# Kernel optimization log

Hardware: AMD Instinct MI355X
Metric: run time of the kernel (lower is better)

The kernel has to match this reference:

```python
import jax, jax.numpy as jnp
import numpy as np

B, N, E, D, STEPS = 32, 512, 4, 128, 5  # batch, n_node, n_edge_types, state_dim, n_steps


def setup_inputs() -> dict:
    key = jax.random.key(0)
    ks = jax.random.split(key, 16)
    s = 0.05  # xavier-ish scale for weights
    inp = {
        "prop_state": jax.random.normal(ks[0], (B, N, D), jnp.float32),
        # dense adjacency [B, N, 2*N*E]; scale by 1/(N) to keep bmm sums O(1)
        "A": jax.random.uniform(ks[1], (B, N, 2 * N * E), jnp.float32) * (2.0 / N),
        "node_mask": jnp.ones((B, N), dtype=jnp.int32),
        # per-edge-type in/out linears (applied orientation: x @ W + b)
        "in_W": jax.random.normal(ks[2], (E, D, D), jnp.float32) * s,
        "in_b": jax.random.normal(ks[3], (E, D), jnp.float32) * 1e-4,
        "out_W": jax.random.normal(ks[4], (E, D, D), jnp.float32) * s,
        "out_b": jax.random.normal(ks[5], (E, D), jnp.float32) * 1e-4,
        # GRU-style gates: Linear(3D -> D)
        "rW": jax.random.normal(ks[6], (3 * D, D), jnp.float32) * s,
        "rb": jax.random.normal(ks[7], (D,), jnp.float32) * 1e-4,
        "zW": jax.random.normal(ks[8], (3 * D, D), jnp.float32) * s,
        "zb": jax.random.normal(ks[9], (D,), jnp.float32) * 1e-4,
        "tW": jax.random.normal(ks[10], (3 * D, D), jnp.float32) * s,
        "tb": jax.random.normal(ks[11], (D,), jnp.float32) * 1e-4,
        # out_mlp: Linear(2D -> D) (dropout p=0 / eval mode -> identity)
        "oW": jax.random.normal(ks[12], (2 * D, D), jnp.float32) * s,
        "ob": jax.random.normal(ks[13], (D,), jnp.float32) * 1e-4,
    }
    return inp


def reference(prop_state, A, node_mask, in_W, in_b, out_W, out_b,
              rW, rb, zW, zb, tW, tb, oW, ob):
    del node_mask  # accepted but unused by GGNN.forward
    init_state = prop_state
    A_in = A[:, :, : N * E]    # [B, N, N*E]
    A_out = A[:, :, N * E:]    # [B, N, N*E]
    state = prop_state         # [B, N, D]
    for _ in range(STEPS):
        # per-edge-type linears, stacked edge-type-major: [B, E, N, D] -> [B, E*N, D]
        in_states = (jnp.einsum('bnd,edh->benh', state, in_W)
                     + in_b[None, :, None, :]).reshape(B, E * N, D)
        out_states = (jnp.einsum('bnd,edh->benh', state, out_W)
                      + out_b[None, :, None, :]).reshape(B, E * N, D)
        a_in = jnp.einsum('bnm,bmd->bnd', A_in, in_states)    # [B, N, D]
        a_out = jnp.einsum('bnm,bmd->bnd', A_out, out_states)  # [B, N, D]
        a = jnp.concatenate([a_in, a_out, state], axis=2)      # [B, N, 3D]
        r = jax.nn.sigmoid(a @ rW + rb)
        z = jax.nn.sigmoid(a @ zW + zb)
        joined = jnp.concatenate([a_in, a_out, r * state], axis=2)
        h_hat = jnp.tanh(joined @ tW + tb)
        state = (1.0 - z) * state + z * h_hat
    join_state = jnp.concatenate([state, init_state], axis=2)  # [B, N, 2D]
    return jnp.tanh(join_state @ oW + ob)                      # [B, N, D]
```

## Files before the change

### kernel.cpp

```cpp
#include <hip/hip_runtime.h>

#define DEV __device__ __forceinline__

using half8   = __attribute__((ext_vector_type(8))) _Float16;
using ushort8 = __attribute__((ext_vector_type(8))) unsigned short;
using f32x4   = __attribute__((ext_vector_type(4))) float;

typedef unsigned short ushort_t;

constexpr int B_ = 32, N_ = 512, E_ = 4, D_ = 128;
constexpr int NE = N_ * E_;
constexpr int M_TOT = B_ * N_;
constexpr int STEPS_ = 5;

DEV ushort_t f2h(float x) { union { _Float16 h; ushort_t u; } v; v.h = (_Float16)x; return v.u; }
DEV float sigmoidf_(float x) { return 1.0f / (1.0f + __expf(-x)); }

template<int ROWS>
DEV void stage64(const ushort_t* __restrict__ g, int ld, ushort_t* lds, int tid) {
    constexpr int TOT = ROWS * 8;
    static_assert(TOT % 256 == 0, "");
    int w = tid >> 6, lane = tid & 63;
#pragma unroll
    for (int c0 = 0; c0 < TOT; c0 += 256) {
        int c  = c0 + (w << 6) + lane;
        int r  = c >> 3;
        int cc = c & 7;
        __builtin_amdgcn_global_load_lds(
            (__attribute__((address_space(1))) void*)(g + r * ld + cc * 8),
            (__attribute__((address_space(3))) void*)(lds + (c0 + (w << 6)) * 8),
            16, 0, 0);
    }
}

template<int BM, int BN>
DEV void mma64(const ushort_t* lA, const ushort_t* lB,
               f32x4 (&acc)[BM/32][BN/32], int wm, int wn, int l15, int lg) {
    constexpr int MF = BM / 32, NF = BN / 32;
#pragma unroll
    for (int kk = 0; kk < 2; ++kk) {
        half8 a[MF], b[NF];
#pragma unroll
        for (int i = 0; i < MF; ++i)
            a[i] = *reinterpret_cast<const half8*>(lA + (wm*(BM/2) + i*16 + l15)*64 + kk*32 + lg*8);
#pragma unroll
        for (int j = 0; j < NF; ++j)
            b[j] = *reinterpret_cast<const half8*>(lB + (wn*(BN/2) + j*16 + l15)*64 + kk*32 + lg*8);
#pragma unroll
        for (int i = 0; i < MF; ++i)
#pragma unroll
            for (int j = 0; j < NF; ++j)
                acc[i][j] = __builtin_amdgcn_mfma_f32_16x16x32_f16(a[i], b[j], acc[i][j], 0, 0, 0);
    }
}

__global__ __launch_bounds__(256) void convertA_rs(const float* __restrict__ A,
                                                   ushort_t* __restrict__ A_h,
                                                   float* __restrict__ Ars) {
    int row = blockIdx.x, t = threadIdx.x;
    const float* src = A + (size_t)row * 4096 + t * 16;
    ushort_t* dst = A_h + (size_t)row * 4096 + t * 16;
    float s = 0.f;
#pragma unroll
    for (int c = 0; c < 2; ++c) {
        float4 v0 = reinterpret_cast<const float4*>(src)[2*c];
        float4 v1 = reinterpret_cast<const float4*>(src)[2*c+1];
        s += v0.x+v0.y+v0.z+v0.w + v1.x+v1.y+v1.z+v1.w;
        ushort8 r;
        r[0]=f2h(v0.x); r[1]=f2h(v0.y); r[2]=f2h(v0.z); r[3]=f2h(v0.w);
        r[4]=f2h(v1.x); r[5]=f2h(v1.y); r[6]=f2h(v1.z); r[7]=f2h(v1.w);
        *reinterpret_cast<ushort8*>(dst + 8*c) = r;
    }
#pragma unroll
    for (int m = 16; m; m >>= 1) s += __shfl_xor(s, m);
    if ((t & 31) == 0) Ars[(size_t)row * 8 + (t >> 5)] = s;
}

__global__ __launch_bounds__(256) void prep_weights(
    const float* __restrict__ in_W, const float* __restrict__ out_W,
    const float* __restrict__ rW, const float* __restrict__ zW,
    const float* __restrict__ tW, const float* __restrict__ oW,
    ushort_t* WstT, ushort_t* WrzT, ushort_t* WtT, ushort_t* WoT) {
    int idx = blockIdx.x * 256 + threadIdx.x;
    if (idx < 131072) {
        int io = idx >> 16, r = idx & 65535, d = r >> 9, eh = r & 511, e = eh >> 7, h = eh & 127;
        const float* W = io ? out_W : in_W;
        WstT[idx] = f2h(W[e*16384 + h*128 + d]);
        return;
    }
    idx -= 131072;
    if (idx < 98304) {
        int j = idx / 384, k = idx % 384;
        WrzT[idx] = f2h(j < 128 ? rW[k*128 + j] : zW[k*128 + (j-128)]);
        return;
    }
    idx -= 98304;
    if (idx < 49152) { int j = idx / 384, k = idx % 384; WtT[idx] = f2h(tW[k*128 + j]); return; }
    idx -= 49152;
    if (idx < 32768) { int j = idx / 256, k = idx % 256; WoT[idx] = f2h(oW[k*128 + j]); return; }
}

__global__ __launch_bounds__(256) void initState(const float* __restrict__ p,
                                                 float* __restrict__ sf,
                                                 ushort_t* __restrict__ sh,
                                                 ushort_t* __restrict__ ih) {
    int i = blockIdx.x * 256 + threadIdx.x;
    float4 v = reinterpret_cast<const float4*>(p)[i];
    reinterpret_cast<float4*>(sf)[i] = v;
    using u4 = __attribute__((ext_vector_type(4))) unsigned short;
    u4 r; r[0]=f2h(v.x); r[1]=f2h(v.y); r[2]=f2h(v.z); r[3]=f2h(v.w);
    *reinterpret_cast<u4*>(sh + 4*i) = r;
    *reinterpret_cast<u4*>(ih + 4*i) = r;
}

__global__ __launch_bounds__(256) void transT_kernel(const ushort_t* __restrict__ sh,
                                                     ushort_t* __restrict__ stateT) {
    __shared__ alignas(16) ushort_t trb[128 * 136];
    int tid = threadIdx.x, b = blockIdx.x >> 2, n0 = (blockIdx.x & 3) * 128;
#pragma unroll
    for (int rep = 0; rep < 8; ++rep) {
        int idx = rep * 256 + tid, r = idx >> 4, c8 = idx & 15;
        uint4 v = *reinterpret_cast<const uint4*>(sh + ((size_t)(b*512 + n0 + r))*128 + c8*8);
        *reinterpret_cast<uint4*>(trb + r*136 + c8*8) = v;
    }
    __syncthreads();
    int d = tid >> 1, half = tid & 1;
    ushort_t* dst = stateT + (size_t)b * 65536 + d * 512 + n0 + half * 64;
#pragma unroll
    for (int g = 0; g < 8; ++g) {
        ushort8 v;
#pragma unroll
        for (int k = 0; k < 8; ++k) v[k] = trb[(half*64 + g*8 + k)*136 + d];
        *reinterpret_cast<ushort8*>(dst + g*8) = v;
    }
}

__global__ __launch_bounds__(256) void bigG_kernel(const ushort_t* __restrict__ A_h,
                                                   const ushort_t* __restrict__ stateT,
                                                   ushort_t* __restrict__ G) {
    __shared__ alignas(16) ushort_t lA[128*64];
    __shared__ alignas(16) ushort_t lB[128*64];
    int tid = threadIdx.x, w = tid >> 6, l15 = tid & 15, lg = (tid & 63) >> 4;
    int wm = w >> 1, wn = w & 1;
    int bx = blockIdx.x;
    int bid = (bx & 7) * 128 + (bx >> 3);
    int nt = bid & 3, e = (bid >> 2) & 3, io = (bid >> 4) & 1, b = bid >> 5;

    const ushort_t* Asrc = A_h + ((size_t)(b*512 + nt*128))*4096 + io*2048 + e*512;
    const ushort_t* Bsrc = stateT + (size_t)b * 65536;
    ushort_t* Out = G + ((size_t)(b*512 + nt*128))*1024 + io*512 + e*128;

    f32x4 acc[4][4] = {};
    for (int k0 = 0; k0 < 512; k0 += 64) {
        stage64<128>(Asrc + k0, 4096, lA, tid);
        stage64<128>(Bsrc + k0, 512, lB, tid);
        __syncthreads();
        mma64<128, 128>(lA, lB, acc, wm, wn, l15, lg);
        __syncthreads();
    }
#pragma unroll
    for (int j = 0; j < 4; ++j) {
        int col = wn*64 + j*16 + l15;
#pragma unroll
        for (int i = 0; i < 4; ++i)
#pragma unroll
            for (int q = 0; q < 4; ++q) {
                int row = wm*64 + i*16 + lg*4 + q;
                Out[(size_t)row * 1024 + col] = f2h(acc[i][j][q]);
            }
    }
}

__global__ __launch_bounds__(256) void applyW_kernel(const ushort_t* __restrict__ G,
                                                     const ushort_t* __restrict__ WstT,
                                                     const float* __restrict__ Ars,
                                                     const float* __restrict__ in_b,
                                                     const float* __restrict__ out_b,
                                                     ushort_t* __restrict__ a_in_h,
                                                     ushort_t* __restrict__ a_out_h) {
    __shared__ alignas(16) ushort_t lA[128*64];
    __shared__ alignas(16) ushort_t lB[128*64];
    int tid = threadIdx.x, w = tid >> 6, l15 = tid & 15, lg = (tid & 63) >> 4;
    int wm = w >> 1, wn = w & 1;
    int mt = blockIdx.x >> 1, io = blockIdx.x & 1;

    const ushort_t* Asrc = G + (size_t)(mt*128)*1024 + io*512;
    const ushort_t* Bsrc = WstT + io * 65536;
    const float* bio = io ? out_b : in_b;
    ushort_t* Out = (io ? a_out_h : a_in_h);

    f32x4 acc[4][4] = {};
    for (int k0 = 0; k0 < 512; k0 += 64) {
        stage64<128>(Asrc + k0, 1024, lA, tid);
        stage64<128>(Bsrc + k0, 512, lB, tid);
        __syncthreads();
        mma64<128, 128>(lA, lB, acc, wm, wn, l15, lg);
        __syncthreads();
    }
#pragma unroll
    for (int j = 0; j < 4; ++j) {
        int col = wn*64 + j*16 + l15;
        float b0 = bio[col], b1 = bio[128+col], b2 = bio[256+col], b3 = bio[384+col];
#pragma unroll
        for (int i = 0; i < 4; ++i)
#pragma unroll
            for (int q = 0; q < 4; ++q) {
                int row = mt*128 + wm*64 + i*16 + lg*4 + q;
                float4 rs = *reinterpret_cast<const float4*>(Ars + (size_t)row*8 + io*4);
                float v = acc[i][j][q] + rs.x*b0 + rs.y*b1 + rs.z*b2 + rs.w*b3;
                Out[(size_t)row * 128 + col] = f2h(v);
            }
    }
}

__global__ __launch_bounds__(256) void rz_kernel(const ushort_t* __restrict__ a_in_h,
                                                 const ushort_t* __restrict__ a_out_h,
                                                 const ushort_t* __restrict__ state_h,
                                                 const ushort_t* __restrict__ WrzT,
                                                 const float* __restrict__ rb,
                                                 const float* __restrict__ zb,
                                                 const float* __restrict__ state_f32,
                                                 ushort_t* __restrict__ rsh,
                                                 float* __restrict__ z_f32) {
    __shared__ alignas(16) ushort_t lA[128*64];
    __shared__ alignas(16) ushort_t lB[128*64];
    int tid = threadIdx.x, w = tid >> 6, l15 = tid & 15, lg = (tid & 63) >> 4;
    int wm = w >> 1, wn = w & 1;
    int mt = blockIdx.x >> 1, cb = blockIdx.x & 1;

    const ushort_t* srcs[3] = { a_in_h + (size_t)mt*128*128,
                                a_out_h + (size_t)mt*128*128,
                                state_h + (size_t)mt*128*128 };
    const ushort_t* Bsrc = WrzT + (size_t)cb * 128 * 384;

    f32x4 acc[4][4] = {};
    for (int k0 = 0; k0 < 384; k0 += 64) {
        stage64<128>(srcs[k0 >> 7] + (k0 & 127), 128, lA, tid);
        stage64<128>(Bsrc + k0, 384, lB, tid);
        __syncthreads();
        mma64<128, 128>(lA, lB, acc, wm, wn, l15, lg);
        __syncthreads();
    }
    const float* bias = cb ? zb : rb;
#pragma unroll
    for (int j = 0; j < 4; ++j) {
        int col = wn*64 + j*16 + l15;
        float bv = bias[col];
#pragma unroll
        for (int i = 0; i < 4; ++i)
#pragma unroll
            for (int q = 0; q < 4; ++q) {
                int row = mt*128 + wm*64 + i*16 + lg*4 + q;
                size_t idx = (size_t)row * 128 + col;
                float g = sigmoidf_(acc[i][j][q] + bv);
                if (cb == 0) rsh[idx] = f2h(g * state_f32[idx]);
                else         z_f32[idx] = g;
            }
    }
}

__global__ __launch_bounds__(256) void t_kernel(const ushort_t* __restrict__ a_in_h,
                                                const ushort_t* __restrict__ a_out_h,
                                                const ushort_t* __restrict__ rsh,
                                                const ushort_t* __restrict__ WtT,
                                                const float* __restrict__ tb,
                                                const float* __restrict__ z_f32,
                                                float* __restrict__ state_f32,
                                                ushort_t* __restrict__ state_h,
                                                ushort_t* __restrict__ stateT) {
    __shared__ alignas(16) ushort_t sbuf[128 * 136];
    ushort_t* lA = sbuf;
    ushort_t* lB = sbuf + 8192;
    int tid = threadIdx.x, w = tid >> 6, l15 = tid & 15, lg = (tid & 63) >> 4;
    int wm = w >> 1, wn = w & 1;
    int mt = blockIdx.x;

    const ushort_t* srcs[3] = { a_in_h + (size_t)mt*128*128,
                                a_out_h + (size_t)mt*128*128,
                                rsh + (size_t)mt*128*128 };
    f32x4 acc[4][4] = {};
    for (int k0 = 0; k0 < 384; k0 += 64) {
        stage64<128>(srcs[k0 >> 7] + (k0 & 127), 128, lA, tid);
        stage64<128>(WtT + k0, 384, lB, tid);
        __syncthreads();
        mma64<128, 128>(lA, lB, acc, wm, wn, l15, lg);
        __syncthreads();
    }
#pragma unroll
    for (int j = 0; j < 4; ++j) {
        int col = wn*64 + j*16 + l15;
        float bv = tb[col];
#pragma unroll
        for (int i = 0; i < 4; ++i)
#pragma unroll
            for (int q = 0; q < 4; ++q) {
                int lrow = wm*64 + i*16 + lg*4 + q;
                int row = mt*128 + lrow;
                size_t idx = (size_t)row * 128 + col;
                float h = tanhf(acc[i][j][q] + bv);
                float z = z_f32[idx];
                float ns = (1.0f - z) * state_f32[idx] + z * h;
                state_f32[idx] = ns;
                ushort_t nh = f2h(ns);
                state_h[idx] = nh;
                sbuf[lrow * 136 + col] = nh;
            }
    }
    __syncthreads();
    int b = mt >> 2, n0 = (mt & 3) * 128;
    int d = tid >> 1, half = tid & 1;
    ushort_t* dst = stateT + (size_t)b * 65536 + d * 512 + n0 + half * 64;
#pragma unroll
    for (int g = 0; g < 8; ++g) {
        ushort8 v;
#pragma unroll
        for (int k = 0; k < 8; ++k) v[k] = sbuf[(half*64 + g*8 + k)*136 + d];
        *reinterpret_cast<ushort8*>(dst + g*8) = v;
    }
}

__global__ __launch_bounds__(256) void final_kernel(const ushort_t* __restrict__ state_h,
                                                    const ushort_t* __restrict__ init_h,
                                                    const ushort_t* __restrict__ WoT,
                                                    const float* __restrict__ ob,
                                                    float* __restrict__ out) {
    __shared__ alignas(16) ushort_t lA[128*64];
    __shared__ alignas(16) ushort_t lB[128*64];
    int tid = threadIdx.x, w = tid >> 6, l15 = tid & 15, lg = (tid & 63) >> 4;
    int wm = w >> 1, wn = w & 1;
    int mt = blockIdx.x;

    const ushort_t* srcs[2] = { state_h + (size_t)mt*128*128,
                                init_h + (size_t)mt*128*128 };
    f32x4 acc[4][4] = {};
    for (int k0 = 0; k0 < 256; k0 += 64) {
        stage64<128>(srcs[k0 >> 7] + (k0 & 127), 128, lA, tid);
        stage64<128>(WoT + k0, 256, lB, tid);
        __syncthreads();
        mma64<128, 128>(lA, lB, acc, wm, wn, l15, lg);
        __syncthreads();
    }
#pragma unroll
    for (int j = 0; j < 4; ++j) {
        int col = wn*64 + j*16 + l15;
        float bv = ob[col];
#pragma unroll
        for (int i = 0; i < 4; ++i)
#pragma unroll
            for (int q = 0; q < 4; ++q) {
                int row = mt*128 + wm*64 + i*16 + lg*4 + q;
                out[(size_t)row * 128 + col] = tanhf(acc[i][j][q] + bv);
            }
    }
}

extern "C" void kernel_launch(void* const* d_in, const int* in_sizes, int n_in,
                              void* d_out, int out_size, void* d_ws, size_t ws_size,
                              hipStream_t stream) {
    const float* prop  = (const float*)d_in[0];
    const float* A     = (const float*)d_in[1];
    const float* in_W  = (const float*)d_in[3];
    const float* in_b  = (const float*)d_in[4];
    const float* out_W = (const float*)d_in[5];
    const float* out_b = (const float*)d_in[6];
    const float* rW    = (const float*)d_in[7];
    const float* rb    = (const float*)d_in[8];
    const float* zW    = (const float*)d_in[9];
    const float* zb    = (const float*)d_in[10];
    const float* tW    = (const float*)d_in[11];
    const float* tb    = (const float*)d_in[12];
    const float* oW    = (const float*)d_in[13];
    const float* ob    = (const float*)d_in[14];
    float* outp = (float*)d_out;

    size_t off = 0;
    auto carve = [&](size_t bytes) {
        void* p = (char*)d_ws + off;
        off += (bytes + 255) & ~(size_t)255;
        return p;
    };
    ushort_t* A_h      = (ushort_t*)carve((size_t)M_TOT*4096*2);
    ushort_t* G        = (ushort_t*)carve((size_t)M_TOT*1024*2);
    ushort_t* stateT   = (ushort_t*)carve((size_t)B_*D_*N_*2);
    ushort_t* a_in_h   = (ushort_t*)carve((size_t)M_TOT*D_*2);
    ushort_t* a_out_h  = (ushort_t*)carve((size_t)M_TOT*D_*2);
    ushort_t* rsh      = (ushort_t*)carve((size_t)M_TOT*D_*2);
    ushort_t* state_h  = (ushort_t*)carve((size_t)M_TOT*D_*2);
    ushort_t* init_h   = (ushort_t*)carve((size_t)M_TOT*D_*2);
    float*    state_f32= (float*)carve((size_t)M_TOT*D_*4);
    float*    z_f32    = (float*)carve((size_t)M_TOT*D_*4);
    float*    Ars      = (float*)carve((size_t)M_TOT*8*4);
    ushort_t* WstT     = (ushort_t*)carve((size_t)2*128*512*2);
    ushort_t* WrzT     = (ushort_t*)carve((size_t)256*384*2);
    ushort_t* WtT      = (ushort_t*)carve((size_t)128*384*2);
    ushort_t* WoT      = (ushort_t*)carve((size_t)128*256*2);
    (void)ws_size; (void)n_in; (void)in_sizes; (void)out_size;

    convertA_rs<<<16384, 256, 0, stream>>>(A, A_h, Ars);
    prep_weights<<<1216, 256, 0, stream>>>(in_W, out_W, rW, zW, tW, oW, WstT, WrzT, WtT, WoT);
    initState<<<2048, 256, 0, stream>>>(prop, state_f32, state_h, init_h);
    transT_kernel<<<128, 256, 0, stream>>>(state_h, stateT);

    for (int s = 0; s < STEPS_; ++s) {
        bigG_kernel<<<1024, 256, 0, stream>>>(A_h, stateT, G);
        applyW_kernel<<<256, 256, 0, stream>>>(G, WstT, Ars, in_b, out_b, a_in_h, a_out_h);
        rz_kernel<<<256, 256, 0, stream>>>(a_in_h, a_out_h, state_h, WrzT, rb, zb,
                                           state_f32, rsh, z_f32);
        t_kernel<<<128, 256, 0, stream>>>(a_in_h, a_out_h, rsh, WtT, tb, z_f32,
                                          state_f32, state_h, stateT);
    }
    final_kernel<<<128, 256, 0, stream>>>(state_h, init_h, WoT, ob, outp);
}
```

Measured before the change: 998.9 us.

## Fuse applyW, rz and t stages into one GRU kernel with LDS-resident intermediates

Merges the per-step applyW, rz and t kernels into a single gru_kernel that handles 64-row tiles. a_in, a_out and r*state stay in swizzled LDS instead of going through global memory, and z is held in registers. It also fuses initState with the transpose, and stages bigG's output through LDS so global stores are coalesced. This cuts launches and global round-trips but uses 72KB of LDS per block, runs only 256 blocks, and has the smaller tile re-read the weight tiles more often.

Result: faster. 832.2 us (-16.7%).

```diff
diff --git a/kernel.cpp b/kernel.cpp
--- a/kernel.cpp
+++ b/kernel.cpp
@@ -33,25 +33,41 @@
     }
 }
 
-template<int BM, int BN>
-DEV void mma64(const ushort_t* lA, const ushort_t* lB,
-               f32x4 (&acc)[BM/32][BN/32], int wm, int wn, int l15, int lg) {
-    constexpr int MF = BM / 32, NF = BN / 32;
+DEV void st_swz(ushort_t* base, int row, int col, ushort_t v) {
+    int off = ((row * 128 + col) * 2) ^ ((row & 7) << 4);
+    *reinterpret_cast<ushort_t*>(reinterpret_cast<char*>(base) + off) = v;
+}
+
+template<int BM, int BN, int LDA, bool SWZ>
+DEV void mmaT(const ushort_t* lA, int k0, const ushort_t* lB,
+              f32x4 (&acc)[BM/32][BN/32], int wm, int wn, int l15, int lg) {
+    constexpr int MF = BM/32, NF = BN/32;
 #pragma unroll
     for (int kk = 0; kk < 2; ++kk) {
         half8 a[MF], b[NF];
 #pragma unroll
-        for (int i = 0; i < MF; ++i)
-            a[i] = *reinterpret_cast<const half8*>(lA + (wm*(BM/2) + i*16 + l15)*64 + kk*32 + lg*8);
+        for (int i = 0; i < MF; ++i) {
+            int row = wm*(BM/2) + i*16 + l15;
+            int off = (row*LDA + k0 + kk*32 + lg*8) * 2;
+            if (SWZ) off ^= (row & 7) << 4;
+            a[i] = *reinterpret_cast<const half8*>(reinterpret_cast<const char*>(lA) + off);
+        }
 #pragma unroll
         for (int j = 0; j < NF; ++j)
-            b[j] = *reinterpret_cast<const half8*>(lB + (wn*(BN/2) + j*16 + l15)*64 + kk*32 + lg*8);
+            b[j] = *reinterpret_cast<const half8*>(lB + (wn*(BN/2)+j*16+l15)*64 + kk*32 + lg*8);
 #pragma unroll
         for (int i = 0; i < MF; ++i)
 #pragma unroll
             for (int j = 0; j < NF; ++j)
                 acc[i][j] = __builtin_amdgcn_mfma_f32_16x16x32_f16(a[i], b[j], acc[i][j], 0, 0, 0);
     }
+}
+
+DEV void zacc(f32x4 (&acc)[2][4]) {
+#pragma unroll
+    for (int i = 0; i < 2; ++i)
+#pragma unroll
+        for (int j = 0; j < 4; ++j) acc[i][j] = (f32x4){0.f,0.f,0.f,0.f};
 }
 
 __global__ __launch_bounds__(256) void convertA_rs(const float* __restrict__ A,
@@ -100,46 +116,46 @@
     if (idx < 32768) { int j = idx / 256, k = idx % 256; WoT[idx] = f2h(oW[k*128 + j]); return; }
 }
 
-__global__ __launch_bounds__(256) void initState(const float* __restrict__ p,
-                                                 float* __restrict__ sf,
-                                                 ushort_t* __restrict__ sh,
-                                                 ushort_t* __restrict__ ih) {
-    int i = blockIdx.x * 256 + threadIdx.x;
-    float4 v = reinterpret_cast<const float4*>(p)[i];
-    reinterpret_cast<float4*>(sf)[i] = v;
-    using u4 = __attribute__((ext_vector_type(4))) unsigned short;
-    u4 r; r[0]=f2h(v.x); r[1]=f2h(v.y); r[2]=f2h(v.z); r[3]=f2h(v.w);
-    *reinterpret_cast<u4*>(sh + 4*i) = r;
-    *reinterpret_cast<u4*>(ih + 4*i) = r;
-}
-
-__global__ __launch_bounds__(256) void transT_kernel(const ushort_t* __restrict__ sh,
-                                                     ushort_t* __restrict__ stateT) {
-    __shared__ alignas(16) ushort_t trb[128 * 136];
-    int tid = threadIdx.x, b = blockIdx.x >> 2, n0 = (blockIdx.x & 3) * 128;
-#pragma unroll
-    for (int rep = 0; rep < 8; ++rep) {
-        int idx = rep * 256 + tid, r = idx >> 4, c8 = idx & 15;
-        uint4 v = *reinterpret_cast<const uint4*>(sh + ((size_t)(b*512 + n0 + r))*128 + c8*8);
-        *reinterpret_cast<uint4*>(trb + r*136 + c8*8) = v;
+__global__ __launch_bounds__(256) void initPlus(const float* __restrict__ p,
+                                                float* __restrict__ sf,
+                                                ushort_t* __restrict__ sh,
+                                                ushort_t* __restrict__ ih,
+                                                ushort_t* __restrict__ stateT) {
+    __shared__ ushort_t trb[128 * 132];
+    int tid = threadIdx.x, mt = blockIdx.x;
+    size_t base = (size_t)mt * 128 * 128;
+#pragma unroll
+    for (int rep = 0; rep < 16; ++rep) {
+        int idx = rep * 256 + tid, row = idx >> 5, c4 = idx & 31;
+        size_t o = base + (size_t)row * 128 + c4 * 4;
+        float4 v = *reinterpret_cast<const float4*>(p + o);
+        *reinterpret_cast<float4*>(sf + o) = v;
+        using u4 = __attribute__((ext_vector_type(4))) unsigned short;
+        u4 r; r[0]=f2h(v.x); r[1]=f2h(v.y); r[2]=f2h(v.z); r[3]=f2h(v.w);
+        *reinterpret_cast<u4*>(sh + o) = r;
+        *reinterpret_cast<u4*>(ih + o) = r;
+        trb[row*132 + c4*4 + 0] = r[0]; trb[row*132 + c4*4 + 1] = r[1];
+        trb[row*132 + c4*4 + 2] = r[2]; trb[row*132 + c4*4 + 3] = r[3];
     }
     __syncthreads();
-    int d = tid >> 1, half = tid & 1;
-    ushort_t* dst = stateT + (size_t)b * 65536 + d * 512 + n0 + half * 64;
-#pragma unroll
-    for (int g = 0; g < 8; ++g) {
+    int b = mt >> 2, n0 = (mt & 3) * 128, d = tid >> 1, half = tid & 1;
+    ushort_t* dst = stateT + (size_t)b * 65536 + (size_t)d * 512 + n0 + half * 64;
+#pragma unroll
+    for (int g2 = 0; g2 < 8; ++g2) {
         ushort8 v;
 #pragma unroll
-        for (int k = 0; k < 8; ++k) v[k] = trb[(half*64 + g*8 + k)*136 + d];
-        *reinterpret_cast<ushort8*>(dst + g*8) = v;
+        for (int k = 0; k < 8; ++k) v[k] = trb[(half*64 + g2*8 + k)*132 + d];
+        *reinterpret_cast<ushort8*>(dst + g2*8) = v;
     }
 }
 
 __global__ __launch_bounds__(256) void bigG_kernel(const ushort_t* __restrict__ A_h,
                                                    const ushort_t* __restrict__ stateT,
                                                    ushort_t* __restrict__ G) {
-    __shared__ alignas(16) ushort_t lA[128*64];
-    __shared__ alignas(16) ushort_t lB[128*64];
+    __shared__ char smem[128*136*2] __attribute__((aligned(16)));
+    ushort_t* sA  = (ushort_t*)smem;
+    ushort_t* sB  = (ushort_t*)(smem + 16384);
+    ushort_t* buf = (ushort_t*)smem;
     int tid = threadIdx.x, w = tid >> 6, l15 = tid & 15, lg = (tid & 63) >> 4;
     int wm = w >> 1, wn = w & 1;
     int bx = blockIdx.x;
@@ -152,10 +168,10 @@
 
     f32x4 acc[4][4] = {};
     for (int k0 = 0; k0 < 512; k0 += 64) {
-        stage64<128>(Asrc + k0, 4096, lA, tid);
-        stage64<128>(Bsrc + k0, 512, lB, tid);
+        stage64<128>(Asrc + k0, 4096, sA, tid);
+        stage64<128>(Bsrc + k0, 512, sB, tid);
         __syncthreads();
-        mma64<128, 128>(lA, lB, acc, wm, wn, l15, lg);
+        mmaT<128, 128, 64, false>(sA, 0, sB, acc, wm, wn, l15, lg);
         __syncthreads();
     }
 #pragma unroll
@@ -166,157 +182,168 @@
 #pragma unroll
             for (int q = 0; q < 4; ++q) {
                 int row = wm*64 + i*16 + lg*4 + q;
-                Out[(size_t)row * 1024 + col] = f2h(acc[i][j][q]);
+                buf[row*136 + col] = f2h(acc[i][j][q]);
             }
     }
-}
-
-__global__ __launch_bounds__(256) void applyW_kernel(const ushort_t* __restrict__ G,
-                                                     const ushort_t* __restrict__ WstT,
-                                                     const float* __restrict__ Ars,
-                                                     const float* __restrict__ in_b,
-                                                     const float* __restrict__ out_b,
-                                                     ushort_t* __restrict__ a_in_h,
-                                                     ushort_t* __restrict__ a_out_h) {
-    __shared__ alignas(16) ushort_t lA[128*64];
-    __shared__ alignas(16) ushort_t lB[128*64];
+    __syncthreads();
+#pragma unroll
+    for (int rep = 0; rep < 8; ++rep) {
+        int idx = rep*256 + tid, row = idx >> 4, c8 = idx & 15;
+        uint4 v = *reinterpret_cast<uint4*>(buf + row*136 + c8*8);
+        *reinterpret_cast<uint4*>(Out + (size_t)row*1024 + c8*8) = v;
+    }
+}
+
+__global__ __launch_bounds__(256, 2) void gru_kernel(
+    const ushort_t* __restrict__ G, const ushort_t* __restrict__ WstT,
+    const float* __restrict__ Ars, const float* __restrict__ in_b,
+    const float* __restrict__ out_b,
+    const ushort_t* __restrict__ WrzT, const float* __restrict__ rb,
+    const float* __restrict__ zb,
+    const ushort_t* __restrict__ WtT, const float* __restrict__ tb,
+    float* __restrict__ state_f32, ushort_t* __restrict__ state_h,
+    ushort_t* __restrict__ stateT) {
+    __shared__ char smem[73728] __attribute__((aligned(16)));
+    ushort_t* sA    = (ushort_t*)smem;
+    ushort_t* sB    = (ushort_t*)(smem + 8192);
+    ushort_t* a_in  = (ushort_t*)(smem + 24576);
+    ushort_t* a_out = (ushort_t*)(smem + 40960);
+    ushort_t* rsb   = (ushort_t*)(smem + 57344);
+    ushort_t* trb   = (ushort_t*)smem;
+
     int tid = threadIdx.x, w = tid >> 6, l15 = tid & 15, lg = (tid & 63) >> 4;
     int wm = w >> 1, wn = w & 1;
-    int mt = blockIdx.x >> 1, io = blockIdx.x & 1;
-
-    const ushort_t* Asrc = G + (size_t)(mt*128)*1024 + io*512;
-    const ushort_t* Bsrc = WstT + io * 65536;
-    const float* bio = io ? out_b : in_b;
-    ushort_t* Out = (io ? a_out_h : a_in_h);
-
-    f32x4 acc[4][4] = {};
-    for (int k0 = 0; k0 < 512; k0 += 64) {
-        stage64<128>(Asrc + k0, 1024, lA, tid);
-        stage64<128>(Bsrc + k0, 512, lB, tid);
-        __syncthreads();
-        mma64<128, 128>(lA, lB, acc, wm, wn, l15, lg);
-        __syncthreads();
-    }
+    int grow0 = blockIdx.x * 64;
+
+    f32x4 acc[2][4];
+    f32x4 zr[2][4];
+
+#define GRU_KSTEP_GLB(APTR, ALD, BPTR, BLD) do {                         \
+        stage64<64>((APTR), (ALD), sA, tid);                             \
+        stage64<128>((BPTR), (BLD), sB, tid);                            \
+        __syncthreads();                                                 \
+        mmaT<64,128,64,false>(sA, 0, sB, acc, wm, wn, l15, lg);          \
+        __syncthreads(); } while (0)
+
+#define GRU_KSTEP_LDS(ABASE, K0, BPTR, BLD) do {                         \
+        stage64<128>((BPTR), (BLD), sB, tid);                            \
+        __syncthreads();                                                 \
+        mmaT<64,128,128,true>((ABASE), (K0), sB, acc, wm, wn, l15, lg);  \
+        __syncthreads(); } while (0)
+
+    for (int io = 0; io < 2; ++io) {
+        zacc(acc);
+        for (int k0 = 0; k0 < 512; k0 += 64) {
+            GRU_KSTEP_GLB(G + (size_t)grow0*1024 + io*512 + k0, 1024,
+                          WstT + io*65536 + k0, 512);
+        }
+        const float* bio = io ? out_b : in_b;
+        ushort_t* adst = io ? a_out : a_in;
+#pragma unroll
+        for (int j = 0; j < 4; ++j) {
+            int col = wn*64 + j*16 + l15;
+            float b0 = bio[col], b1 = bio[128+col], b2 = bio[256+col], b3 = bio[384+col];
+#pragma unroll
+            for (int i = 0; i < 2; ++i)
+#pragma unroll
+                for (int q = 0; q < 4; ++q) {
+                    int row = wm*32 + i*16 + lg*4 + q;
+                    float4 rsv = *reinterpret_cast<const float4*>(Ars + (size_t)(grow0+row)*8 + io*4);
+                    float v = acc[i][j][q] + rsv.x*b0 + rsv.y*b1 + rsv.z*b2 + rsv.w*b3;
+                    st_swz(adst, row, col, f2h(v));
+                }
+        }
+    }
+
+    zacc(acc);
+    GRU_KSTEP_LDS(a_in,  0,  WrzT + 0,   384);
+    GRU_KSTEP_LDS(a_in,  64, WrzT + 64,  384);
+    GRU_KSTEP_LDS(a_out, 0,  WrzT + 128, 384);
+    GRU_KSTEP_LDS(a_out, 64, WrzT + 192, 384);
+    GRU_KSTEP_GLB(state_h + (size_t)grow0*128,      128, WrzT + 256, 384);
+    GRU_KSTEP_GLB(state_h + (size_t)grow0*128 + 64, 128, WrzT + 320, 384);
 #pragma unroll
     for (int j = 0; j < 4; ++j) {
         int col = wn*64 + j*16 + l15;
-        float b0 = bio[col], b1 = bio[128+col], b2 = bio[256+col], b3 = bio[384+col];
-#pragma unroll
-        for (int i = 0; i < 4; ++i)
+        float rbv = rb[col];
+#pragma unroll
+        for (int i = 0; i < 2; ++i)
 #pragma unroll
             for (int q = 0; q < 4; ++q) {
-                int row = mt*128 + wm*64 + i*16 + lg*4 + q;
-                float4 rs = *reinterpret_cast<const float4*>(Ars + (size_t)row*8 + io*4);
-                float v = acc[i][j][q] + rs.x*b0 + rs.y*b1 + rs.z*b2 + rs.w*b3;
-                Out[(size_t)row * 128 + col] = f2h(v);
+                int row = wm*32 + i*16 + lg*4 + q;
+                size_t idx = (size_t)(grow0+row)*128 + col;
+                float rg = sigmoidf_(acc[i][j][q] + rbv);
+                st_swz(rsb, row, col, f2h(rg * state_f32[idx]));
             }
     }
-}
-
-__global__ __launch_bounds__(256) void rz_kernel(const ushort_t* __restrict__ a_in_h,
-                                                 const ushort_t* __restrict__ a_out_h,
-                                                 const ushort_t* __restrict__ state_h,
-                                                 const ushort_t* __restrict__ WrzT,
-                                                 const float* __restrict__ rb,
-                                                 const float* __restrict__ zb,
-                                                 const float* __restrict__ state_f32,
-                                                 ushort_t* __restrict__ rsh,
-                                                 float* __restrict__ z_f32) {
-    __shared__ alignas(16) ushort_t lA[128*64];
-    __shared__ alignas(16) ushort_t lB[128*64];
-    int tid = threadIdx.x, w = tid >> 6, l15 = tid & 15, lg = (tid & 63) >> 4;
-    int wm = w >> 1, wn = w & 1;
-    int mt = blockIdx.x >> 1, cb = blockIdx.x & 1;
-
-    const ushort_t* srcs[3] = { a_in_h + (size_t)mt*128*128,
-                                a_out_h + (size_t)mt*128*128,
-                                state_h + (size_t)mt*128*128 };
-    const ushort_t* Bsrc = WrzT + (size_t)cb * 128 * 384;
-
-    f32x4 acc[4][4] = {};
-    for (int k0 = 0; k0 < 384; k0 += 64) {
-        stage64<128>(srcs[k0 >> 7] + (k0 & 127), 128, lA, tid);
-        stage64<128>(Bsrc + k0, 384, lB, tid);
-        __syncthreads();
-        mma64<128, 128>(lA, lB, acc, wm, wn, l15, lg);
-        __syncthreads();
-    }
-    const float* bias = cb ? zb : rb;
+
+    zacc(acc);
+    {
+        const ushort_t* Wz = WrzT + 128*384;
+        GRU_KSTEP_LDS(a_in,  0,  Wz + 0,   384);
+        GRU_KSTEP_LDS(a_in,  64, Wz + 64,  384);
+        GRU_KSTEP_LDS(a_out, 0,  Wz + 128, 384);
+        GRU_KSTEP_LDS(a_out, 64, Wz + 192, 384);
+        GRU_KSTEP_GLB(state_h + (size_t)grow0*128,      128, Wz + 256, 384);
+        GRU_KSTEP_GLB(state_h + (size_t)grow0*128 + 64, 128, Wz + 320, 384);
+    }
 #pragma unroll
     for (int j = 0; j < 4; ++j) {
         int col = wn*64 + j*16 + l15;
-        float bv = bias[col];
-#pragma unroll
-        for (int i = 0; i < 4; ++i)
-#pragma unroll
-            for (int q = 0; q < 4; ++q) {
-                int row = mt*128 + wm*64 + i*16 + lg*4 + q;
-                size_t idx = (size_t)row * 128 + col;
-                float g = sigmoidf_(acc[i][j][q] + bv);
-                if (cb == 0) rsh[idx] = f2h(g * state_f32[idx]);
-                else         z_f32[idx] = g;
-            }
-    }
-}
-
-__global__ __launch_bounds__(256) void t_kernel(const ushort_t* __restrict__ a_in_h,
-                                                const ushort_t* __restrict__ a_out_h,
-                                                const ushort_t* __restrict__ rsh,
-                                                const ushort_t* __restrict__ WtT,
-                                                const float* __restrict__ tb,
-                                                const float* __restrict__ z_f32,
-                                                float* __restrict__ state_f32,
-                                                ushort_t* __restrict__ state_h,
-                                                ushort_t* __restrict__ stateT) {
-    __shared__ alignas(16) ushort_t sbuf[128 * 136];
-    ushort_t* lA = sbuf;
-    ushort_t* lB = sbuf + 8192;
-    int tid = threadIdx.x, w = tid >> 6, l15 = tid & 15, lg = (tid & 63) >> 4;
-    int wm = w >> 1, wn = w & 1;
-    int mt = blockIdx.x;
-
-    const ushort_t* srcs[3] = { a_in_h + (size_t)mt*128*128,
-                                a_out_h + (size_t)mt*128*128,
-                                rsh + (size_t)mt*128*128 };
-    f32x4 acc[4][4] = {};
-    for (int k0 = 0; k0 < 384; k0 += 64) {
-        stage64<128>(srcs[k0 >> 7] + (k0 & 127), 128, lA, tid);
-        stage64<128>(WtT + k0, 384, lB, tid);
-        __syncthreads();
-        mma64<128, 128>(lA, lB, acc, wm, wn, l15, lg);
-        __syncthreads();
-    }
+        float zbv = zb[col];
+#pragma unroll
+        for (int i = 0; i < 2; ++i)
+#pragma unroll
+            for (int q = 0; q < 4; ++q)
+                zr[i][j][q] = sigmoidf_(acc[i][j][q] + zbv);
+    }
+
+    zacc(acc);
+    GRU_KSTEP_LDS(a_in,  0,  WtT + 0,   384);
+    GRU_KSTEP_LDS(a_in,  64, WtT + 64,  384);
+    GRU_KSTEP_LDS(a_out, 0,  WtT + 128, 384);
+    GRU_KSTEP_LDS(a_out, 64, WtT + 192, 384);
+    GRU_KSTEP_LDS(rsb,   0,  WtT + 256, 384);
+    GRU_KSTEP_LDS(rsb,   64, WtT + 320, 384);
 #pragma unroll
     for (int j = 0; j < 4; ++j) {
         int col = wn*64 + j*16 + l15;
-        float bv = tb[col];
-#pragma unroll
-        for (int i = 0; i < 4; ++i)
+        float tbv = tb[col];
+#pragma unroll
+        for (int i = 0; i < 2; ++i)
 #pragma unroll
             for (int q = 0; q < 4; ++q) {
-                int lrow = wm*64 + i*16 + lg*4 + q;
-                int row = mt*128 + lrow;
-                size_t idx = (size_t)row * 128 + col;
-                float h = tanhf(acc[i][j][q] + bv);
-                float z = z_f32[idx];
+                int row = wm*32 + i*16 + lg*4 + q;
+                size_t idx = (size_t)(grow0+row)*128 + col;
+                float h = tanhf(acc[i][j][q] + tbv);
+                float z = zr[i][j][q];
                 float ns = (1.0f - z) * state_f32[idx] + z * h;
                 state_f32[idx] = ns;
-                ushort_t nh = f2h(ns);
-                state_h[idx] = nh;
-                sbuf[lrow * 136 + col] = nh;
+                trb[row*132 + col] = f2h(ns);
             }
     }
     __syncthreads();
-    int b = mt >> 2, n0 = (mt & 3) * 128;
-    int d = tid >> 1, half = tid & 1;
-    ushort_t* dst = stateT + (size_t)b * 65536 + d * 512 + n0 + half * 64;
-#pragma unroll
-    for (int g = 0; g < 8; ++g) {
+#pragma unroll
+    for (int rep = 0; rep < 4; ++rep) {
+        int idx = rep*256 + tid, row = idx >> 4, c8 = idx & 15;
         ushort8 v;
 #pragma unroll
-        for (int k = 0; k < 8; ++k) v[k] = sbuf[(half*64 + g*8 + k)*136 + d];
-        *reinterpret_cast<ushort8*>(dst + g*8) = v;
-    }
+        for (int k = 0; k < 8; ++k) v[k] = trb[row*132 + c8*8 + k];
+        *reinterpret_cast<ushort8*>(state_h + (size_t)(grow0+row)*128 + c8*8) = v;
+    }
+    {
+        int b = grow0 >> 9, n0 = grow0 & 511, d = tid >> 1, half = tid & 1;
+        ushort_t* dst = stateT + (size_t)b*65536 + (size_t)d*512 + n0 + half*32;
+#pragma unroll
+        for (int g2 = 0; g2 < 4; ++g2) {
+            ushort8 v;
+#pragma unroll
+            for (int k = 0; k < 8; ++k) v[k] = trb[(half*32 + g2*8 + k)*132 + d];
+            *reinterpret_cast<ushort8*>(dst + g2*8) = v;
+        }
+    }
+#undef GRU_KSTEP_GLB
+#undef GRU_KSTEP_LDS
 }
 
 __global__ __launch_bounds__(256) void final_kernel(const ushort_t* __restrict__ state_h,
@@ -337,7 +364,7 @@
         stage64<128>(srcs[k0 >> 7] + (k0 & 127), 128, lA, tid);
         stage64<128>(WoT + k0, 256, lB, tid);
         __syncthreads();
-        mma64<128, 128>(lA, lB, acc, wm, wn, l15, lg);
+        mmaT<128, 128, 64, false>(lA, 0, lB, acc, wm, wn, l15, lg);
         __syncthreads();
     }
 #pragma unroll
@@ -382,13 +409,9 @@
     ushort_t* A_h      = (ushort_t*)carve((size_t)M_TOT*4096*2);
     ushort_t* G        = (ushort_t*)carve((size_t)M_TOT*1024*2);
     ushort_t* stateT   = (ushort_t*)carve((size_t)B_*D_*N_*2);
-    ushort_t* a_in_h   = (ushort_t*)carve((size_t)M_TOT*D_*2);
-    ushort_t* a_out_h  = (ushort_t*)carve((size_t)M_TOT*D_*2);
-    ushort_t* rsh      = (ushort_t*)carve((size_t)M_TOT*D_*2);
     ushort_t* state_h  = (ushort_t*)carve((size_t)M_TOT*D_*2);
     ushort_t* init_h   = (ushort_t*)carve((size_t)M_TOT*D_*2);
     float*    state_f32= (float*)carve((size_t)M_TOT*D_*4);
-    float*    z_f32    = (float*)carve((size_t)M_TOT*D_*4);
     float*    Ars      = (float*)carve((size_t)M_TOT*8*4);
     ushort_t* WstT     = (ushort_t*)carve((size_t)2*128*512*2);
     ushort_t* WrzT     = (ushort_t*)carve((size_t)256*384*2);
@@ -398,16 +421,13 @@
 
     convertA_rs<<<16384, 256, 0, stream>>>(A, A_h, Ars);
     prep_weights<<<1216, 256, 0, stream>>>(in_W, out_W, rW, zW, tW, oW, WstT, WrzT, WtT, WoT);
-    initState<<<2048, 256, 0, stream>>>(prop, state_f32, state_h, init_h);
-    transT_kernel<<<128, 256, 0, stream>>>(state_h, stateT);
+    initPlus<<<128, 256, 0, stream>>>(prop, state_f32, state_h, init_h, stateT);
 
     for (int s = 0; s < STEPS_; ++s) {
         bigG_kernel<<<1024, 256, 0, stream>>>(A_h, stateT, G);
-        applyW_kernel<<<256, 256, 0, stream>>>(G, WstT, Ars, in_b, out_b, a_in_h, a_out_h);
-        rz_kernel<<<256, 256, 0, stream>>>(a_in_h, a_out_h, state_h, WrzT, rb, zb,
-                                           state_f32, rsh, z_f32);
-        t_kernel<<<128, 256, 0, stream>>>(a_in_h, a_out_h, rsh, WtT, tb, z_f32,
-                                          state_f32, state_h, stateT);
+        gru_kernel<<<256, 256, 0, stream>>>(G, WstT, Ars, in_b, out_b,
+                                            WrzT, rb, zb, WtT, tb,
+                                            state_f32, state_h, stateT);
     }
     final_kernel<<<128, 256, 0, stream>>>(state_h, init_h, WoT, ob, outp);
 }
```
